# Kernel tuning notes

Measured on AMD Instinct MI355X. Metric: run time of the kernel, lower is better.

The kernel has to match this reference:

```python
import jax, jax.numpy as jnp
import numpy as np

N = 50000        # nodes
E = 800000       # edges (avg degree 16)
D_IN = 128
D_OUT = 128
P_DROP = 0.1
BN_EPS = 1e-5


def setup_inputs() -> dict:
    key = jax.random.key(0)
    k1, k2, k3 = jax.random.split(key, 3)
    x = jax.random.normal(k1, (N, D_IN), dtype=jnp.float32)
    edge_index = jax.random.randint(k2, (2, E), 0, N, dtype=jnp.int64)
    W = jax.random.normal(k3, (D_IN, D_OUT), dtype=jnp.float32) / np.sqrt(D_IN).astype(np.float32)
    b = jnp.zeros((D_OUT,), jnp.float32)
    bn_gamma = jnp.ones((D_OUT,), jnp.float32)
    bn_beta = jnp.zeros((D_OUT,), jnp.float32)
    return {"x": x, "edge_index": edge_index, "W": W, "b": b,
            "bn_gamma": bn_gamma, "bn_beta": bn_beta}


def reference(x, edge_index, W, b, bn_gamma, bn_beta):
    n = x.shape[0]
    # --- GCNConv: h = x W, symmetric-normalized aggregation with self-loops ---
    h = x @ W                                            # [N, D_OUT]
    loops = jnp.arange(n, dtype=edge_index.dtype)
    src = jnp.concatenate([edge_index[0], loops])        # [E+N]
    dst = jnp.concatenate([edge_index[1], loops])        # [E+N]
    deg = jax.ops.segment_sum(jnp.ones_like(dst, h.dtype), dst, num_segments=n)
    dinv = jax.lax.rsqrt(jnp.maximum(deg, 1.0))          # deg >= 1 (self-loops)
    norm = dinv[src] * dinv[dst]                         # [E+N]
    msg = h[src] * norm[:, None]                         # gather + weight
    z = jax.ops.segment_sum(msg, dst, num_segments=n) + b
    # --- activation ---
    z = jax.nn.relu(z)
    # --- BatchNorm over nodes (training-mode batch statistics) ---
    mean = z.mean(axis=0)
    var = z.var(axis=0)
    z = bn_gamma * (z - mean) * jax.lax.rsqrt(var + BN_EPS) + bn_beta
    # --- dropout (training mode, fixed key for determinism) ---
    keep = jax.random.bernoulli(jax.random.key(42), 1.0 - P_DROP, z.shape)
    z = jnp.where(keep, z / (1.0 - P_DROP), 0.0)
    return z.astype(x.dtype)
```

## Files before the change

kernel.cpp:

```cpp
#include <hip/hip_runtime.h>
#include <stdint.h>


#define NN 50000
#define NE 800000
#define DD 128
#define SCAN_B 256
#define NSB ((NN + SCAN_B - 1) / SCAN_B)
#define NSTAT 400

using f32x4  = __attribute__((ext_vector_type(4))) float;
using short8 = __attribute__((ext_vector_type(8))) short;

__device__ __forceinline__ uint32_t rotl32(uint32_t x, uint32_t d) {
  return (x << d) | (x >> (32u - d));
}

__device__ __forceinline__ uint32_t threefry_bits(uint32_t idx) {
  const uint32_t ks0 = 0u;
  const uint32_t ks1 = 42u;
  const uint32_t ks2 = 0x1BD11BDAu ^ ks0 ^ ks1;
  uint32_t x0 = ks0;
  uint32_t x1 = idx + ks1;
#define TF_R(r) { x0 += x1; x1 = rotl32(x1, (r)); x1 ^= x0; }
  TF_R(13u) TF_R(15u) TF_R(26u) TF_R(6u)
  x0 += ks1; x1 += ks2 + 1u;
  TF_R(17u) TF_R(29u) TF_R(16u) TF_R(24u)
  x0 += ks2; x1 += ks0 + 2u;
  TF_R(13u) TF_R(15u) TF_R(26u) TF_R(6u)
  x0 += ks0; x1 += ks1 + 3u;
  TF_R(17u) TF_R(29u) TF_R(16u) TF_R(24u)
  x0 += ks1; x1 += ks2 + 4u;
  TF_R(13u) TF_R(15u) TF_R(26u) TF_R(6u)
  x0 += ks2; x1 += ks0 + 5u;
#undef TF_R
  return x0 ^ x1;
}

__device__ __forceinline__ uint32_t f2bf(float f) {
  uint32_t u = __float_as_uint(f);
  return (u + 0x7fffu + ((u >> 16) & 1u)) >> 16;
}
__device__ __forceinline__ float bf2f(uint32_t h) { return __uint_as_float(h << 16); }
__device__ __forceinline__ float bf_lo(uint32_t p) { return __uint_as_float(p << 16); }
__device__ __forceinline__ float bf_hi(uint32_t p) { return __uint_as_float(p & 0xffff0000u); }

__global__ __launch_bounds__(256) void k_wpack(const float* __restrict__ Wm,
                                               short8* __restrict__ wfh,
                                               short8* __restrict__ wfl) {
  int tid = blockIdx.x * 256 + threadIdx.x;
  if (tid >= 32 * 64) return;
  int lane = tid & 63;
  int cfks = tid >> 6;
  int ks = cfks >> 3, cf = cfks & 7;
  int krow = ks * 32 + ((lane >> 4) << 3);
  int col = cf * 16 + (lane & 15);
  short8 h, l;
#pragma unroll
  for (int j = 0; j < 8; ++j) {
    float w = Wm[(size_t)(krow + j) * DD + col];
    uint32_t hb = f2bf(w);
    uint32_t lb = f2bf(w - bf2f(hb));
    h[j] = (short)hb;
    l[j] = (short)lb;
  }
  wfh[tid] = h;
  wfl[tid] = l;
}

#define GBM 128
__global__ __launch_bounds__(256) void k_gemm(const float* __restrict__ x,
                                              const short8* __restrict__ wfh,
                                              const short8* __restrict__ wfl,
                                              uint16_t* __restrict__ hbf) {
  __shared__ uint4 ldsbuf[4096];
  char* lds = (char*)ldsbuf;
  const int t = threadIdx.x;
  const int row0 = blockIdx.x * GBM;
  const int c4 = t & 31, rbase = t >> 5;

#pragma unroll
  for (int i = 0; i < 16; ++i) {
    int r = rbase + i * 8;
    int grow = row0 + r;
    float4 v = make_float4(0.f, 0.f, 0.f, 0.f);
    if (grow < NN)
      v = *reinterpret_cast<const float4*>(&x[(size_t)grow * DD + c4 * 4]);
    uint32_t h0 = f2bf(v.x), h1 = f2bf(v.y), h2 = f2bf(v.z), h3 = f2bf(v.w);
    uint32_t l0 = f2bf(v.x - bf2f(h0)), l1 = f2bf(v.y - bf2f(h1));
    uint32_t l2 = f2bf(v.z - bf2f(h2)), l3 = f2bf(v.w - bf2f(h3));
    int byte = (r * 256 + c4 * 8) ^ ((r & 7) << 4);
    *reinterpret_cast<uint2*>(lds + byte) = make_uint2(h0 | (h1 << 16), h2 | (h3 << 16));
    *reinterpret_cast<uint2*>(lds + 32768 + byte) = make_uint2(l0 | (l1 << 16), l2 | (l3 << 16));
  }
  __syncthreads();

  const int wv = t >> 6, l = t & 63;
  f32x4 acc[2][8] = {};
#pragma unroll
  for (int ks = 0; ks < 4; ++ks) {
    short8 ah[2], al[2];
#pragma unroll
    for (int rf = 0; rf < 2; ++rf) {
      int r = wv * 32 + rf * 16 + (l & 15);
      int byte = (r * 256 + ks * 64 + ((l >> 4) << 4)) ^ ((r & 7) << 4);
      ah[rf] = *reinterpret_cast<const short8*>(lds + byte);
      al[rf] = *reinterpret_cast<const short8*>(lds + 32768 + byte);
    }
#pragma unroll
    for (int cf = 0; cf < 8; ++cf) {
      short8 bh = wfh[(ks * 8 + cf) * 64 + l];
      short8 bl = wfl[(ks * 8 + cf) * 64 + l];
#pragma unroll
      for (int rf = 0; rf < 2; ++rf) {
        acc[rf][cf] = __builtin_amdgcn_mfma_f32_16x16x32_bf16(ah[rf], bl, acc[rf][cf], 0, 0, 0);
        acc[rf][cf] = __builtin_amdgcn_mfma_f32_16x16x32_bf16(al[rf], bh, acc[rf][cf], 0, 0, 0);
        acc[rf][cf] = __builtin_amdgcn_mfma_f32_16x16x32_bf16(ah[rf], bh, acc[rf][cf], 0, 0, 0);
      }
    }
  }
  __syncthreads();

#pragma unroll
  for (int rf = 0; rf < 2; ++rf)
#pragma unroll
    for (int cf = 0; cf < 8; ++cf)
#pragma unroll
      for (int i = 0; i < 4; ++i) {
        int row = wv * 32 + rf * 16 + ((l >> 4) << 2) + i;
        int col = cf * 16 + (l & 15);
        int byte = (row * 256 + col * 2) ^ ((row & 7) << 4);
        *reinterpret_cast<uint16_t*>(lds + byte) = (uint16_t)f2bf(acc[rf][cf][i]);
      }
  __syncthreads();
#pragma unroll
  for (int i = 0; i < 16; ++i) {
    int r = rbase + i * 8;
    int grow = row0 + r;
    if (grow < NN) {
      int byte = (r * 256 + c4 * 8) ^ ((r & 7) << 4);
      uint2 v = *reinterpret_cast<const uint2*>(lds + byte);
      *reinterpret_cast<uint2*>(&hbf[(size_t)grow * DD + c4 * 4]) = v;
    }
  }
}

__global__ void k_count(const int* __restrict__ ei, int* __restrict__ cnt,
                        int* __restrict__ pos) {
  int e = blockIdx.x * blockDim.x + threadIdx.x;
  if (e < NE) pos[e] = atomicAdd(&cnt[ei[NE + e]], 1);
}

__global__ __launch_bounds__(SCAN_B) void k_scan1(const int* __restrict__ cnt,
                                                  int* __restrict__ tmp,
                                                  int* __restrict__ blk_sums) {
  __shared__ int sm[SCAN_B];
  int t = threadIdx.x;
  int i = blockIdx.x * SCAN_B + t;
  int v = (i < NN) ? cnt[i] : 0;
  sm[t] = v;
  __syncthreads();
  for (int off = 1; off < SCAN_B; off <<= 1) {
    int u = (t >= off) ? sm[t - off] : 0;
    __syncthreads();
    sm[t] += u;
    __syncthreads();
  }
  if (i < NN) tmp[i] = sm[t];
  if (t == SCAN_B - 1) blk_sums[blockIdx.x] = sm[t];
}

__global__ __launch_bounds__(SCAN_B) void k_scan2(const int* __restrict__ blk_sums,
                                                  int* __restrict__ blk_off) {
  __shared__ int sm[SCAN_B];
  int t = threadIdx.x;
  int v = (t < NSB) ? blk_sums[t] : 0;
  sm[t] = v;
  __syncthreads();
  for (int off = 1; off < SCAN_B; off <<= 1) {
    int u = (t >= off) ? sm[t - off] : 0;
    __syncthreads();
    sm[t] += u;
    __syncthreads();
  }
  if (t < NSB) blk_off[t] = sm[t] - v;
}

__global__ void k_scan3(const int* __restrict__ tmp, const int* __restrict__ blk_off,
                        const int* __restrict__ cnt, int* __restrict__ row_ptr,
                        float* __restrict__ dinv) {
  int i = blockIdx.x * SCAN_B + threadIdx.x;
  if (i < NN) {
    row_ptr[i + 1] = tmp[i] + blk_off[i >> 8];
    if (i == 0) row_ptr[0] = 0;
    dinv[i] = rsqrtf((float)cnt[i] + 1.0f);
  }
}

__global__ void k_fill(const int* __restrict__ ei, const int* __restrict__ row_ptr,
                       const int* __restrict__ pos, int* __restrict__ colv) {
  int e = blockIdx.x * blockDim.x + threadIdx.x;
  if (e < NE) {
    int d = ei[NE + e];
    colv[row_ptr[d] + pos[e]] = ei[e];
  }
}

__global__ __launch_bounds__(256) void k_agg(const uint16_t* __restrict__ hbf,
                                             const int* __restrict__ row_ptr,
                                             const int* __restrict__ colv,
                                             const float* __restrict__ dinv,
                                             const float* __restrict__ bias,
                                             float* __restrict__ z) {
  int wave = threadIdx.x >> 6;
  int lane = threadIdx.x & 63;
  int node = blockIdx.x * 4 + wave;
  if (node >= NN) return;
  const uint32_t* hp = reinterpret_cast<const uint32_t*>(hbf);

  float di = dinv[node];
  float w0 = di * di;
  uint32_t ms = hp[(size_t)node * 64 + lane];
  float ax = bf_lo(ms) * w0, ay = bf_hi(ms) * w0;

  int e = row_ptr[node], end = row_ptr[node + 1];
  while (e + 8 <= end) {
    int s[8]; float w[8]; uint32_t m[8];
#pragma unroll
    for (int q = 0; q < 8; ++q) s[q] = colv[e + q];
#pragma unroll
    for (int q = 0; q < 8; ++q) { w[q] = dinv[s[q]]; m[q] = hp[(size_t)s[q] * 64 + lane]; }
#pragma unroll
    for (int q = 0; q < 8; ++q) {
      float wq = w[q] * di;
      ax = fmaf(bf_lo(m[q]), wq, ax);
      ay = fmaf(bf_hi(m[q]), wq, ay);
    }
    e += 8;
  }
  while (e < end) {
    int s0 = colv[e];
    float wq = dinv[s0] * di;
    uint32_t m0 = hp[(size_t)s0 * 64 + lane];
    ax = fmaf(bf_lo(m0), wq, ax);
    ay = fmaf(bf_hi(m0), wq, ay);
    ++e;
  }
  float2 bb = reinterpret_cast<const float2*>(bias)[lane];
  float zx = fmaxf(ax + bb.x, 0.f);
  float zy = fmaxf(ay + bb.y, 0.f);
  reinterpret_cast<float2*>(z)[(size_t)node * 64 + lane] = make_float2(zx, zy);
}

__global__ __launch_bounds__(256) void k_stats(const float* __restrict__ z,
                                               float* __restrict__ part) {
  int t = threadIdx.x;
  int c4 = t & 31;
  int rgrp = t >> 5;
  float sx = 0.f, sy = 0.f, sz = 0.f, sw = 0.f;
  float qx = 0.f, qy = 0.f, qz = 0.f, qw = 0.f;
  for (int r = blockIdx.x * 8 + rgrp; r < NN; r += NSTAT * 8) {
    float4 v = *reinterpret_cast<const float4*>(&z[(size_t)r * DD + c4 * 4]);
    sx += v.x; sy += v.y; sz += v.z; sw += v.w;
    qx = fmaf(v.x, v.x, qx); qy = fmaf(v.y, v.y, qy);
    qz = fmaf(v.z, v.z, qz); qw = fmaf(v.w, v.w, qw);
  }
  __shared__ float sm[2048], sm2[2048];
  sm[t * 4 + 0] = sx; sm[t * 4 + 1] = sy; sm[t * 4 + 2] = sz; sm[t * 4 + 3] = sw;
  sm2[t * 4 + 0] = qx; sm2[t * 4 + 1] = qy; sm2[t * 4 + 2] = qz; sm2[t * 4 + 3] = qw;
  __syncthreads();
  int c = t & 127;
  float acc = 0.f;
  if (t < 128) {
#pragma unroll
    for (int g = 0; g < 8; ++g) acc += sm[g * 128 + c];
  } else {
#pragma unroll
    for (int g = 0; g < 8; ++g) acc += sm2[g * 128 + c];
  }
  part[blockIdx.x * 256 + t] = acc;
}

__global__ __launch_bounds__(256) void k_stats2(const float* __restrict__ part,
                                                float* __restrict__ bn_sum,
                                                float* __restrict__ bn_sumsq) {
  int t = threadIdx.x;
  float acc = 0.f;
  for (int b = 0; b < NSTAT; ++b) acc += part[b * 256 + t];
  if (t < 128) bn_sum[t] = acc;
  else bn_sumsq[t - 128] = acc;
}

__global__ __launch_bounds__(256) void k_final(float* __restrict__ z,
                                               const float* __restrict__ bn_sum,
                                               const float* __restrict__ bn_sumsq,
                                               const float* __restrict__ gamma,
                                               const float* __restrict__ beta) {
  int j4 = blockIdx.x * blockDim.x + threadIdx.x;
  if (j4 >= NN * DD / 4) return;
  int c4 = j4 & 31;
  const float invN = 1.0f / (float)NN;
  float4 s = *reinterpret_cast<const float4*>(&bn_sum[c4 * 4]);
  float4 q = *reinterpret_cast<const float4*>(&bn_sumsq[c4 * 4]);
  float4 g = *reinterpret_cast<const float4*>(&gamma[c4 * 4]);
  float4 bt = *reinterpret_cast<const float4*>(&beta[c4 * 4]);
  float4 v = *reinterpret_cast<const float4*>(&z[(size_t)j4 * 4]);
  float out[4];
  float mm[4] = {s.x * invN, s.y * invN, s.z * invN, s.w * invN};
  float qq[4] = {q.x * invN, q.y * invN, q.z * invN, q.w * invN};
  float gg[4] = {g.x, g.y, g.z, g.w};
  float bb[4] = {bt.x, bt.y, bt.z, bt.w};
  float vv[4] = {v.x, v.y, v.z, v.w};
#pragma unroll
  for (int i = 0; i < 4; ++i) {
    float var = qq[i] - mm[i] * mm[i];
    float rs = rsqrtf(var + 1e-5f);
    float val = (vv[i] - mm[i]) * rs * gg[i] + bb[i];
    uint32_t bits = threefry_bits((uint32_t)(j4 * 4 + i));
    float u = __uint_as_float((bits >> 9) | 0x3f800000u) - 1.0f;
    out[i] = (u < 0.9f) ? val * (1.0f / 0.9f) : 0.0f;
  }
  *reinterpret_cast<float4*>(&z[(size_t)j4 * 4]) = make_float4(out[0], out[1], out[2], out[3]);
}

extern "C" void kernel_launch(void* const* d_in, const int* in_sizes, int n_in,
                              void* d_out, int out_size, void* d_ws, size_t ws_size,
                              hipStream_t stream) {
  const float* x     = (const float*)d_in[0];
  const int*   ei    = (const int*)d_in[1];
  const float* Wm    = (const float*)d_in[2];
  const float* bvec  = (const float*)d_in[3];
  const float* gamma = (const float*)d_in[4];
  const float* beta  = (const float*)d_in[5];
  float* zout = (float*)d_out;

  uint16_t* hbf  = (uint16_t*)d_ws;
  short8* wfh    = (short8*)(hbf + (size_t)NN * DD);
  short8* wfl    = wfh + 2048;
  int* colv      = (int*)(wfl + 2048);
  int* pos       = colv + NE;
  int* cnt       = pos + NE;
  float* bn_sum  = (float*)(cnt + NN);
  float* bn_sumsq= bn_sum + DD;
  int* tmp_scan  = (int*)(bn_sumsq + DD);
  int* row_ptr   = tmp_scan + NN;
  float* dinv    = (float*)(row_ptr + NN + 1);
  int* blk_sums  = (int*)(dinv + NN);
  int* blk_off   = blk_sums + NSB;
  float* part    = (float*)(blk_off + NSB);

  hipMemsetAsync(cnt, 0, (size_t)NN * sizeof(int), stream);

  k_wpack<<<8, 256, 0, stream>>>(Wm, wfh, wfl);
  k_gemm<<<(NN + GBM - 1) / GBM, 256, 0, stream>>>(x, wfh, wfl, hbf);
  k_count<<<(NE + 255) / 256, 256, 0, stream>>>(ei, cnt, pos);
  k_scan1<<<NSB, SCAN_B, 0, stream>>>(cnt, tmp_scan, blk_sums);
  k_scan2<<<1, SCAN_B, 0, stream>>>(blk_sums, blk_off);
  k_scan3<<<NSB, SCAN_B, 0, stream>>>(tmp_scan, blk_off, cnt, row_ptr, dinv);
  k_fill<<<(NE + 255) / 256, 256, 0, stream>>>(ei, row_ptr, pos, colv);
  k_agg<<<(NN + 3) / 4, 256, 0, stream>>>(hbf, row_ptr, colv, dinv, bvec, zout);
  k_stats<<<NSTAT, 256, 0, stream>>>(zout, part);
  k_stats2<<<1, 256, 0, stream>>>(part, bn_sum, bn_sumsq);
  k_final<<<(NN * DD / 4 + 255) / 256, 256, 0, stream>>>(zout, bn_sum, bn_sumsq, gamma, beta);
}
```

Baseline: 163.6 us.

## Replicate degree counters and split aggregation edges across half-waves

Degree counting now spreads atomics over 8 replicated counter arrays chosen by block index, with a per-node prefix over replicas used when filling the CSR column array. The aggregation kernel has each half-wave handle alternating edges and load 8 bytes per lane instead of 4, then combines the halves with a cross-lane shuffle before bias and ReLU. The aim is to cut atomic contention and double the number of outstanding gathers per wave. The cost is a larger counter buffer and memset, an extra prefix array, and idle half-wave lanes on odd-degree tails and at the store.

After: 176.7 us. 8.0% more time.

```diff
diff --git a/kernel.cpp b/kernel.cpp
--- a/kernel.cpp
+++ b/kernel.cpp
@@ -145,20 +145,36 @@
   }
 }
 
-__global__ void k_count(const int* __restrict__ ei, int* __restrict__ cnt,
+__global__ void k_count(const int* __restrict__ ei, int* __restrict__ cntrep,
                         int* __restrict__ pos) {
   int e = blockIdx.x * blockDim.x + threadIdx.x;
-  if (e < NE) pos[e] = atomicAdd(&cnt[ei[NE + e]], 1);
-}
-
-__global__ __launch_bounds__(SCAN_B) void k_scan1(const int* __restrict__ cnt,
+  if (e < NE) {
+    int r = blockIdx.x & 7;
+    pos[e] = atomicAdd(&cntrep[r * NN + ei[NE + e]], 1);
+  }
+}
+
+__global__ __launch_bounds__(SCAN_B) void k_scan1(const int* __restrict__ cntrep,
+                                                  int* __restrict__ prefix,
+                                                  int* __restrict__ cnttot,
                                                   int* __restrict__ tmp,
                                                   int* __restrict__ blk_sums) {
   __shared__ int sm[SCAN_B];
   int t = threadIdx.x;
   int i = blockIdx.x * SCAN_B + t;
-  int v = (i < NN) ? cnt[i] : 0;
-  sm[t] = v;
+  int tot = 0;
+  if (i < NN) {
+    int acc = 0;
+#pragma unroll
+    for (int r = 0; r < 8; ++r) {
+      int c = cntrep[r * NN + i];
+      prefix[r * NN + i] = acc;
+      acc += c;
+    }
+    tot = acc;
+    cnttot[i] = tot;
+  }
+  sm[t] = tot;
   __syncthreads();
   for (int off = 1; off < SCAN_B; off <<= 1) {
     int u = (t >= off) ? sm[t - off] : 0;
@@ -187,22 +203,24 @@
 }
 
 __global__ void k_scan3(const int* __restrict__ tmp, const int* __restrict__ blk_off,
-                        const int* __restrict__ cnt, int* __restrict__ row_ptr,
+                        const int* __restrict__ cnttot, int* __restrict__ row_ptr,
                         float* __restrict__ dinv) {
   int i = blockIdx.x * SCAN_B + threadIdx.x;
   if (i < NN) {
     row_ptr[i + 1] = tmp[i] + blk_off[i >> 8];
     if (i == 0) row_ptr[0] = 0;
-    dinv[i] = rsqrtf((float)cnt[i] + 1.0f);
+    dinv[i] = rsqrtf((float)cnttot[i] + 1.0f);
   }
 }
 
 __global__ void k_fill(const int* __restrict__ ei, const int* __restrict__ row_ptr,
-                       const int* __restrict__ pos, int* __restrict__ colv) {
+                       const int* __restrict__ prefix, const int* __restrict__ pos,
+                       int* __restrict__ colv) {
   int e = blockIdx.x * blockDim.x + threadIdx.x;
   if (e < NE) {
     int d = ei[NE + e];
-    colv[row_ptr[d] + pos[e]] = ei[e];
+    int r = (e >> 8) & 7;
+    colv[row_ptr[d] + prefix[r * NN + d] + pos[e]] = ei[e];
   }
 }
 
@@ -214,42 +232,70 @@
                                              float* __restrict__ z) {
   int wave = threadIdx.x >> 6;
   int lane = threadIdx.x & 63;
+  int half = lane >> 5;
+  int l2 = lane & 31;
   int node = blockIdx.x * 4 + wave;
   if (node >= NN) return;
-  const uint32_t* hp = reinterpret_cast<const uint32_t*>(hbf);
+  const uint2* hp = reinterpret_cast<const uint2*>(hbf);
 
   float di = dinv[node];
-  float w0 = di * di;
-  uint32_t ms = hp[(size_t)node * 64 + lane];
-  float ax = bf_lo(ms) * w0, ay = bf_hi(ms) * w0;
-
-  int e = row_ptr[node], end = row_ptr[node + 1];
-  while (e + 8 <= end) {
-    int s[8]; float w[8]; uint32_t m[8];
-#pragma unroll
-    for (int q = 0; q < 8; ++q) s[q] = colv[e + q];
-#pragma unroll
-    for (int q = 0; q < 8; ++q) { w[q] = dinv[s[q]]; m[q] = hp[(size_t)s[q] * 64 + lane]; }
+  float w0 = di * di * 0.5f;
+  uint2 ms = hp[(size_t)node * 32 + l2];
+  float a0 = bf_lo(ms.x) * w0, a1 = bf_hi(ms.x) * w0;
+  float a2 = bf_lo(ms.y) * w0, a3 = bf_hi(ms.y) * w0;
+
+  int beg = row_ptr[node], end = row_ptr[node + 1];
+  int len = end - beg;
+  int npairs = len >> 1;
+  int p = 0;
+  while (p + 8 <= npairs) {
+    int s[8]; float w[8]; uint2 m[8];
+#pragma unroll
+    for (int q = 0; q < 8; ++q) s[q] = colv[beg + 2 * (p + q) + half];
+#pragma unroll
+    for (int q = 0; q < 8; ++q) { w[q] = dinv[s[q]]; m[q] = hp[(size_t)s[q] * 32 + l2]; }
 #pragma unroll
     for (int q = 0; q < 8; ++q) {
       float wq = w[q] * di;
-      ax = fmaf(bf_lo(m[q]), wq, ax);
-      ay = fmaf(bf_hi(m[q]), wq, ay);
+      a0 = fmaf(bf_lo(m[q].x), wq, a0);
+      a1 = fmaf(bf_hi(m[q].x), wq, a1);
+      a2 = fmaf(bf_lo(m[q].y), wq, a2);
+      a3 = fmaf(bf_hi(m[q].y), wq, a3);
     }
-    e += 8;
-  }
-  while (e < end) {
-    int s0 = colv[e];
+    p += 8;
+  }
+  while (p < npairs) {
+    int s0 = colv[beg + 2 * p + half];
     float wq = dinv[s0] * di;
-    uint32_t m0 = hp[(size_t)s0 * 64 + lane];
-    ax = fmaf(bf_lo(m0), wq, ax);
-    ay = fmaf(bf_hi(m0), wq, ay);
-    ++e;
-  }
-  float2 bb = reinterpret_cast<const float2*>(bias)[lane];
-  float zx = fmaxf(ax + bb.x, 0.f);
-  float zy = fmaxf(ay + bb.y, 0.f);
-  reinterpret_cast<float2*>(z)[(size_t)node * 64 + lane] = make_float2(zx, zy);
+    uint2 m0 = hp[(size_t)s0 * 32 + l2];
+    a0 = fmaf(bf_lo(m0.x), wq, a0);
+    a1 = fmaf(bf_hi(m0.x), wq, a1);
+    a2 = fmaf(bf_lo(m0.y), wq, a2);
+    a3 = fmaf(bf_hi(m0.y), wq, a3);
+    ++p;
+  }
+  if ((len & 1) && half == 0) {
+    int s0 = colv[end - 1];
+    float wq = dinv[s0] * di;
+    uint2 m0 = hp[(size_t)s0 * 32 + l2];
+    a0 = fmaf(bf_lo(m0.x), wq, a0);
+    a1 = fmaf(bf_hi(m0.x), wq, a1);
+    a2 = fmaf(bf_lo(m0.y), wq, a2);
+    a3 = fmaf(bf_hi(m0.y), wq, a3);
+  }
+  a0 += __shfl_xor(a0, 32);
+  a1 += __shfl_xor(a1, 32);
+  a2 += __shfl_xor(a2, 32);
+  a3 += __shfl_xor(a3, 32);
+  if (half == 0) {
+    float4 bb = reinterpret_cast<const float4*>(bias)[l2];
+    float4 out;
+    out.x = fmaxf(a0 + bb.x, 0.f);
+    out.y = fmaxf(a1 + bb.y, 0.f);
+    out.z = fmaxf(a2 + bb.z, 0.f);
+    out.w = fmaxf(a3 + bb.w, 0.f);
+    reinterpret_cast<float4*>(z)[(size_t)node * 32 + l2] = out;
+  }
 }
 
 __global__ __launch_bounds__(256) void k_stats(const float* __restrict__ z,
@@ -339,8 +385,10 @@
   short8* wfl    = wfh + 2048;
   int* colv      = (int*)(wfl + 2048);
   int* pos       = colv + NE;
-  int* cnt       = pos + NE;
-  float* bn_sum  = (float*)(cnt + NN);
+  int* cntrep    = pos + NE;
+  int* cnttot    = cntrep + 8 * NN;
+  int* prefix    = cnttot + NN;
+  float* bn_sum  = (float*)(prefix + 8 * NN);
   float* bn_sumsq= bn_sum + DD;
   int* tmp_scan  = (int*)(bn_sumsq + DD);
   int* row_ptr   = tmp_scan + NN;
@@ -349,15 +397,15 @@
   int* blk_off   = blk_sums + NSB;
   float* part    = (float*)(blk_off + NSB);
 
-  hipMemsetAsync(cnt, 0, (size_t)NN * sizeof(int), stream);
+  hipMemsetAsync(cntrep, 0, (size_t)(8 * NN) * sizeof(int), stream);
 
   k_wpack<<<8, 256, 0, stream>>>(Wm, wfh, wfl);
   k_gemm<<<(NN + GBM - 1) / GBM, 256, 0, stream>>>(x, wfh, wfl, hbf);
-  k_count<<<(NE + 255) / 256, 256, 0, stream>>>(ei, cnt, pos);
-  k_scan1<<<NSB, SCAN_B, 0, stream>>>(cnt, tmp_scan, blk_sums);
+  k_count<<<(NE + 255) / 256, 256, 0, stream>>>(ei, cntrep, pos);
+  k_scan1<<<NSB, SCAN_B, 0, stream>>>(cntrep, prefix, cnttot, tmp_scan, blk_sums);
   k_scan2<<<1, SCAN_B, 0, stream>>>(blk_sums, blk_off);
-  k_scan3<<<NSB, SCAN_B, 0, stream>>>(tmp_scan, blk_off, cnt, row_ptr, dinv);
-  k_fill<<<(NE + 255) / 256, 256, 0, stream>>>(ei, row_ptr, pos, colv);
+  k_scan3<<<NSB, SCAN_B, 0, stream>>>(tmp_scan, blk_off, cnttot, row_ptr, dinv);
+  k_fill<<<(NE + 255) / 256, 256, 0, stream>>>(ei, row_ptr, prefix, pos, colv);
   k_agg<<<(NN + 3) / 4, 256, 0, stream>>>(hbf, row_ptr, colv, dinv, bvec, zout);
   k_stats<<<NSTAT, 256, 0, stream>>>(zout, part);
   k_stats2<<<1, 256, 0, stream>>>(part, bn_sum, bn_sumsq);
```

## Fold source-side degree normalization into GEMM epilogue and merge scan kernels

Applied to the files above, without the earlier changes.

The symmetric normalization is factored so each row of h is pre-scaled by dinv[src] in the GEMM epilogue, and the destination factor is applied once per node after aggregation. This removes the per-edge random gather of dinv[src] and the per-edge multiply from the aggregation loop. The GEMM is moved after the degree computation, dinv is computed in the first scan pass, and the single-block second scan is folded into the third scan kernel, so each block redundantly rescans the block sums. Storing pre-scaled values in bf16 changes rounding slightly.

Result: no change. 163.2 us (-0.3%).

```diff
diff --git a/kernel.cpp b/kernel.cpp
--- a/kernel.cpp
+++ b/kernel.cpp
@@ -72,6 +72,7 @@
 __global__ __launch_bounds__(256) void k_gemm(const float* __restrict__ x,
                                               const short8* __restrict__ wfh,
                                               const short8* __restrict__ wfl,
+                                              const float* __restrict__ dinv,
                                               uint16_t* __restrict__ hbf) {
   __shared__ uint4 ldsbuf[4096];
   char* lds = (char*)ldsbuf;
@@ -124,14 +125,17 @@
 #pragma unroll
   for (int rf = 0; rf < 2; ++rf)
 #pragma unroll
-    for (int cf = 0; cf < 8; ++cf)
-#pragma unroll
-      for (int i = 0; i < 4; ++i) {
-        int row = wv * 32 + rf * 16 + ((l >> 4) << 2) + i;
+    for (int i = 0; i < 4; ++i) {
+      int row = wv * 32 + rf * 16 + ((l >> 4) << 2) + i;
+      int grow = row0 + row;
+      float dv = (grow < NN) ? dinv[grow] : 0.f;
+#pragma unroll
+      for (int cf = 0; cf < 8; ++cf) {
         int col = cf * 16 + (l & 15);
         int byte = (row * 256 + col * 2) ^ ((row & 7) << 4);
-        *reinterpret_cast<uint16_t*>(lds + byte) = (uint16_t)f2bf(acc[rf][cf][i]);
+        *reinterpret_cast<uint16_t*>(lds + byte) = (uint16_t)f2bf(acc[rf][cf][i] * dv);
       }
+    }
   __syncthreads();
 #pragma unroll
   for (int i = 0; i < 16; ++i) {
@@ -153,11 +157,13 @@
 
 __global__ __launch_bounds__(SCAN_B) void k_scan1(const int* __restrict__ cnt,
                                                   int* __restrict__ tmp,
-                                                  int* __restrict__ blk_sums) {
+                                                  int* __restrict__ blk_sums,
+                                                  float* __restrict__ dinv) {
   __shared__ int sm[SCAN_B];
   int t = threadIdx.x;
   int i = blockIdx.x * SCAN_B + t;
   int v = (i < NN) ? cnt[i] : 0;
+  if (i < NN) dinv[i] = rsqrtf((float)v + 1.0f);
   sm[t] = v;
   __syncthreads();
   for (int off = 1; off < SCAN_B; off <<= 1) {
@@ -170,8 +176,9 @@
   if (t == SCAN_B - 1) blk_sums[blockIdx.x] = sm[t];
 }
 
-__global__ __launch_bounds__(SCAN_B) void k_scan2(const int* __restrict__ blk_sums,
-                                                  int* __restrict__ blk_off) {
+__global__ __launch_bounds__(SCAN_B) void k_scan3(const int* __restrict__ tmp,
+                                                  const int* __restrict__ blk_sums,
+                                                  int* __restrict__ row_ptr) {
   __shared__ int sm[SCAN_B];
   int t = threadIdx.x;
   int v = (t < NSB) ? blk_sums[t] : 0;
@@ -183,17 +190,11 @@
     sm[t] += u;
     __syncthreads();
   }
-  if (t < NSB) blk_off[t] = sm[t] - v;
-}
-
-__global__ void k_scan3(const int* __restrict__ tmp, const int* __restrict__ blk_off,
-                        const int* __restrict__ cnt, int* __restrict__ row_ptr,
-                        float* __restrict__ dinv) {
-  int i = blockIdx.x * SCAN_B + threadIdx.x;
+  int excl = sm[blockIdx.x] - blk_sums[blockIdx.x];
+  int i = blockIdx.x * SCAN_B + t;
   if (i < NN) {
-    row_ptr[i + 1] = tmp[i] + blk_off[i >> 8];
+    row_ptr[i + 1] = tmp[i] + excl;
     if (i == 0) row_ptr[0] = 0;
-    dinv[i] = rsqrtf((float)cnt[i] + 1.0f);
   }
 }
 
@@ -218,37 +219,33 @@
   if (node >= NN) return;
   const uint32_t* hp = reinterpret_cast<const uint32_t*>(hbf);
 
-  float di = dinv[node];
-  float w0 = di * di;
   uint32_t ms = hp[(size_t)node * 64 + lane];
-  float ax = bf_lo(ms) * w0, ay = bf_hi(ms) * w0;
+  float ax = bf_lo(ms), ay = bf_hi(ms);
 
   int e = row_ptr[node], end = row_ptr[node + 1];
   while (e + 8 <= end) {
-    int s[8]; float w[8]; uint32_t m[8];
+    int s[8]; uint32_t m[8];
 #pragma unroll
     for (int q = 0; q < 8; ++q) s[q] = colv[e + q];
 #pragma unroll
-    for (int q = 0; q < 8; ++q) { w[q] = dinv[s[q]]; m[q] = hp[(size_t)s[q] * 64 + lane]; }
+    for (int q = 0; q < 8; ++q) m[q] = hp[(size_t)s[q] * 64 + lane];
 #pragma unroll
     for (int q = 0; q < 8; ++q) {
-      float wq = w[q] * di;
-      ax = fmaf(bf_lo(m[q]), wq, ax);
-      ay = fmaf(bf_hi(m[q]), wq, ay);
+      ax += bf_lo(m[q]);
+      ay += bf_hi(m[q]);
     }
     e += 8;
   }
   while (e < end) {
-    int s0 = colv[e];
-    float wq = dinv[s0] * di;
-    uint32_t m0 = hp[(size_t)s0 * 64 + lane];
-    ax = fmaf(bf_lo(m0), wq, ax);
-    ay = fmaf(bf_hi(m0), wq, ay);
+    uint32_t m0 = hp[(size_t)colv[e] * 64 + lane];
+    ax += bf_lo(m0);
+    ay += bf_hi(m0);
     ++e;
   }
+  float di = dinv[node];
   float2 bb = reinterpret_cast<const float2*>(bias)[lane];
-  float zx = fmaxf(ax + bb.x, 0.f);
-  float zy = fmaxf(ay + bb.y, 0.f);
+  float zx = fmaxf(fmaf(ax, di, bb.x), 0.f);
+  float zy = fmaxf(fmaf(ay, di, bb.y), 0.f);
   reinterpret_cast<float2*>(z)[(size_t)node * 64 + lane] = make_float2(zx, zy);
 }
 
@@ -346,17 +343,15 @@
   int* row_ptr   = tmp_scan + NN;
   float* dinv    = (float*)(row_ptr + NN + 1);
   int* blk_sums  = (int*)(dinv + NN);
-  int* blk_off   = blk_sums + NSB;
-  float* part    = (float*)(blk_off + NSB);
+  float* part    = (float*)(blk_sums + NSB);
 
   hipMemsetAsync(cnt, 0, (size_t)NN * sizeof(int), stream);
 
   k_wpack<<<8, 256, 0, stream>>>(Wm, wfh, wfl);
-  k_gemm<<<(NN + GBM - 1) / GBM, 256, 0, stream>>>(x, wfh, wfl, hbf);
   k_count<<<(NE + 255) / 256, 256, 0, stream>>>(ei, cnt, pos);
-  k_scan1<<<NSB, SCAN_B, 0, stream>>>(cnt, tmp_scan, blk_sums);
-  k_scan2<<<1, SCAN_B, 0, stream>>>(blk_sums, blk_off);
-  k_scan3<<<NSB, SCAN_B, 0, stream>>>(tmp_scan, blk_off, cnt, row_ptr, dinv);
+  k_scan1<<<NSB, SCAN_B, 0, stream>>>(cnt, tmp_scan, blk_sums, dinv);
+  k_scan3<<<NSB, SCAN_B, 0, stream>>>(tmp_scan, blk_sums, row_ptr);
+  k_gemm<<<(NN + GBM - 1) / GBM, 256, 0, stream>>>(x, wfh, wfl, dinv, hbf);
   k_fill<<<(NE + 255) / 256, 256, 0, stream>>>(ei, row_ptr, pos, colv);
   k_agg<<<(NN + 3) / 4, 256, 0, stream>>>(hbf, row_ptr, colv, dinv, bvec, zout);
   k_stats<<<NSTAT, 256, 0, stream>>>(zout, part);
```
